# Performance work log

Hardware: AMD Instinct MI355X
Metric: run time of the kernel (lower is better)

The kernel has to match this reference:

```python
import jax, jax.numpy as jnp
import numpy as np

N_NODES = 100000
N_EDGES = 1600000
IN_F, HID_F, OUT_F = 128, 128, 64


def _sage_conv(x, src, dst, W_self, W_neigh, b, n_nodes):
    # DGL SAGEConv 'mean': out = x @ W_self + mean_{u in N(v)} x_u @ W_neigh + b
    agg = jax.ops.segment_sum(x[src], dst, num_segments=n_nodes)  # [N, d]
    deg = jax.ops.segment_sum(jnp.ones_like(dst, dtype=x.dtype), dst, num_segments=n_nodes)
    neigh = agg / jnp.maximum(deg, 1.0)[:, None]  # zero-in-degree nodes -> 0
    return x @ W_self + neigh @ W_neigh + b


def setup_inputs() -> dict:
    key = jax.random.key(0)
    ks = jax.random.split(key, 8)
    return {
        "features": jax.random.normal(ks[0], (N_NODES, IN_F), dtype=jnp.float32),
        "edge_src": jax.random.randint(ks[1], (N_EDGES,), 0, N_NODES, dtype=jnp.int32),
        "edge_dst": jax.random.randint(ks[2], (N_EDGES,), 0, N_NODES, dtype=jnp.int32),
        "W1_self": jax.random.normal(ks[3], (IN_F, HID_F), dtype=jnp.float32) / np.sqrt(IN_F),
        "W1_neigh": jax.random.normal(ks[4], (IN_F, HID_F), dtype=jnp.float32) / np.sqrt(IN_F),
        "b1": jnp.zeros((HID_F,), dtype=jnp.float32),
        "W2_self": jax.random.normal(ks[5], (HID_F, OUT_F), dtype=jnp.float32) / np.sqrt(HID_F),
        "W2_neigh": jax.random.normal(ks[6], (HID_F, OUT_F), dtype=jnp.float32) / np.sqrt(HID_F),
        "b2": jnp.zeros((OUT_F,), dtype=jnp.float32),
    }


def reference(features, edge_src, edge_dst, W1_self, W1_neigh, b1, W2_self, W2_neigh, b2):
    n = features.shape[0]
    x = _sage_conv(features, edge_src, edge_dst, W1_self, W1_neigh, b1, n)
    x = jax.nn.relu(x)
    # dropout with training=False is a no-op
    return _sage_conv(x, edge_src, edge_dst, W2_self, W2_neigh, b2, n)
```

## Files before the change

### kernel.cpp

```cpp
#include <hip/hip_runtime.h>

#define NODES 100000
#define EDGES 1600000
#define BSH 8
#define NBUCK ((NODES + 255) >> BSH)
#define CHUNK 4096
#define LMAX 8192
#define MCHUNKS ((NODES + 31) / 32)

using bf16x8 = __attribute__((ext_vector_type(8))) short;
using f32x4  = __attribute__((ext_vector_type(4))) float;
using f32x2  = __attribute__((ext_vector_type(2))) float;

__device__ __forceinline__ unsigned short f2b(float f) {
    unsigned u = __builtin_bit_cast(unsigned, f);
    unsigned r = (u + 0x7FFFu + ((u >> 16) & 1u)) >> 16;
    return (unsigned short)r;
}

__device__ __forceinline__ f32x2 pkadd(f32x2 a, f32x2 b) {
    f32x2 d;
    asm("v_pk_add_f32 %0, %1, %2" : "=v"(d) : "v"(a), "v"(b));
    return d;
}
__device__ __forceinline__ f32x2 pkfma(f32x2 a, f32x2 b, f32x2 c) {
    f32x2 d;
    asm("v_pk_fma_f32 %0, %1, %2, %3" : "=v"(d) : "v"(a), "v"(b), "v"(c));
    return d;
}
__device__ __forceinline__ unsigned cvt2bf(float lo, float hi) {
    unsigned r;
    asm("v_cvt_pk_bf16_f32 %0, %1, %2" : "=v"(r) : "v"(lo), "v"(hi));
    return r;
}

__device__ __forceinline__ void addpk8(f32x2* a, uint2 v) {
    a[0] = pkadd(a[0], __builtin_amdgcn_cvt_pk_f32_fp8((int)v.x, false));
    a[1] = pkadd(a[1], __builtin_amdgcn_cvt_pk_f32_fp8((int)v.x, true));
    a[2] = pkadd(a[2], __builtin_amdgcn_cvt_pk_f32_fp8((int)v.y, false));
    a[3] = pkadd(a[3], __builtin_amdgcn_cvt_pk_f32_fp8((int)v.y, true));
}


__global__ __launch_bounds__(256) void bhist_kernel(const int* __restrict__ dst,
                                                    int* __restrict__ bucket_cnt) {
    __shared__ int lcnt[512];
    int t = threadIdx.x;
    lcnt[t] = 0; lcnt[t + 256] = 0;
    __syncthreads();
    int base = blockIdx.x * 16384;
    int n = EDGES - base;
    if (n > 16384) n = 16384;
    const int4* d4 = reinterpret_cast<const int4*>(dst + base);
    for (int i = t; i < (n >> 2); i += 256) {
        int4 d = d4[i];
        atomicAdd(&lcnt[d.x >> BSH], 1);
        atomicAdd(&lcnt[d.y >> BSH], 1);
        atomicAdd(&lcnt[d.z >> BSH], 1);
        atomicAdd(&lcnt[d.w >> BSH], 1);
    }
    for (int i = (n & ~3) + t; i < n; i += 256) atomicAdd(&lcnt[dst[base + i] >> BSH], 1);
    __syncthreads();
    if (lcnt[t]) atomicAdd(&bucket_cnt[t], lcnt[t]);
    if (lcnt[t + 256]) atomicAdd(&bucket_cnt[t + 256], lcnt[t + 256]);
}

__global__ void bscan_kernel(const int* __restrict__ bucket_cnt, int* __restrict__ bucket_off,
                             int* __restrict__ gcursor, int* __restrict__ row_ptr) {
    __shared__ int sh[512];
    int t = threadIdx.x;
    int v = (t < NBUCK) ? bucket_cnt[t] : 0;
    sh[t] = v;
    __syncthreads();
    for (int off = 1; off < 512; off <<= 1) {
        int x = (t >= off) ? sh[t - off] : 0;
        __syncthreads();
        sh[t] += x;
        __syncthreads();
    }
    int excl = sh[t] - v;
    if (t < NBUCK) { bucket_off[t] = excl; gcursor[t] = excl; }
    if (t == NBUCK) bucket_off[t] = EDGES;
    if (t == 0) row_ptr[NODES] = EDGES;
}

__global__ __launch_bounds__(256) void binscat_kernel(
    const int* __restrict__ src, const int* __restrict__ dst,
    int* __restrict__ gcursor, unsigned* __restrict__ pairs) {
    __shared__ int cnt[512];
    __shared__ int scn[512];
    __shared__ int gbs[512];
    __shared__ int cur[512];
    __shared__ uint2 stage[CHUNK];
    int t = threadIdx.x;
    int base = blockIdx.x * CHUNK;
    int n = EDGES - base;
    if (n > CHUNK) n = CHUNK;

    cnt[t] = 0; cnt[t + 256] = 0;
    __syncthreads();

    uint2 my[16];
#pragma unroll
    for (int i = 0; i < 16; ++i) {
        int idx = t + i * 256;
        if (idx < n) {
            int d = dst[base + idx];
            int s = src[base + idx];
            my[i] = make_uint2((unsigned)d, (unsigned)s);
            atomicAdd(&cnt[d >> BSH], 1);
        } else {
            my[i] = make_uint2(0xFFFFFFFFu, 0);
        }
    }
    __syncthreads();
    scn[t] = cnt[t]; scn[t + 256] = cnt[t + 256];
    __syncthreads();
    for (int off = 1; off < 512; off <<= 1) {
        int a0 = (t >= off) ? scn[t - off] : 0;
        int a1 = (t + 256 >= off) ? scn[t + 256 - off] : 0;
        __syncthreads();
        scn[t] += a0; scn[t + 256] += a1;
        __syncthreads();
    }
    cur[t] = scn[t] - cnt[t];
    cur[t + 256] = scn[t + 256] - cnt[t + 256];
    __syncthreads();
#pragma unroll
    for (int i = 0; i < 16; ++i) {
        if (my[i].x != 0xFFFFFFFFu) {
            int b = (int)(my[i].x >> BSH);
            int p = atomicAdd(&cur[b], 1);
            stage[p] = my[i];
        }
    }
    for (int b2 = t; b2 < 512; b2 += 256) {
        int c = cnt[b2];
        gbs[b2] = (c > 0 && b2 < NBUCK) ? atomicAdd(&gcursor[b2], c) : 0;
    }
    __syncthreads();
    for (int idx = t; idx < n; idx += 256) {
        uint2 p = stage[idx];
        int b = (int)(p.x >> BSH);
        int excl = scn[b] - cnt[b];
        pairs[gbs[b] + idx - excl] = ((p.x & 255u) << 24) | p.y;
    }
}

__global__ __launch_bounds__(256) void localsort_kernel(
    const unsigned* __restrict__ pairs, const int* __restrict__ bucket_off,
    int* __restrict__ row_ptr, int* __restrict__ src_sorted) {
    __shared__ int cnt[256];
    __shared__ int cur[256];
    __shared__ int stage[LMAX];
    int b = blockIdx.x;
    int t = threadIdx.x;
    int node0 = b << BSH;
    int pbeg = bucket_off[b], pend = bucket_off[b + 1];
    int n = pend - pbeg;
    cnt[t] = 0;
    __syncthreads();
    for (int e = pbeg + t; e < pend; e += 256)
        atomicAdd(&cnt[(int)(pairs[e] >> 24)], 1);
    __syncthreads();
    int v = cnt[t];
    cur[t] = v;
    __syncthreads();
    for (int off = 1; off < 256; off <<= 1) {
        int x = (t >= off) ? cur[t - off] : 0;
        __syncthreads();
        cur[t] += x;
        __syncthreads();
    }
    int excl = cur[t] - v;
    int node = node0 + t;
    if (node < NODES) row_ptr[node] = pbeg + excl;
    cur[t] = excl;
    __syncthreads();
    if (n <= LMAX) {
        for (int e = pbeg + t; e < pend; e += 256) {
            unsigned p = pairs[e];
            int pos = atomicAdd(&cur[(int)(p >> 24)], 1);
            stage[pos] = (int)(p & 0xFFFFFFu);
        }
        __syncthreads();
        for (int i = t; i < n; i += 256) src_sorted[pbeg + i] = stage[i];
    } else {
        for (int e = pbeg + t; e < pend; e += 256) {
            unsigned p = pairs[e];
            int pos = atomicAdd(&cur[(int)(p >> 24)], 1);
            src_sorted[pbeg + pos] = (int)(p & 0xFFFFFFu);
        }
    }
}


__global__ void conv_kernel(const float* __restrict__ in, unsigned short* __restrict__ outb,
                            unsigned char* __restrict__ outq, int n4,
                            const float* __restrict__ W1s, const float* __restrict__ W1n,
                            const float* __restrict__ W2s, const float* __restrict__ W2n,
                            unsigned short* __restrict__ Wt1s, unsigned short* __restrict__ Wt1n,
                            unsigned short* __restrict__ Wt2s, unsigned short* __restrict__ Wt2n) {
    int i = blockIdx.x * 256 + threadIdx.x;
    if (i < n4) {
        float4 v = reinterpret_cast<const float4*>(in)[i];
        uint2 o;
        o.x = (unsigned)f2b(v.x) | ((unsigned)f2b(v.y) << 16);
        o.y = (unsigned)f2b(v.z) | ((unsigned)f2b(v.w) << 16);
        reinterpret_cast<uint2*>(outb)[i] = o;
        int pk = __builtin_amdgcn_cvt_pk_fp8_f32(v.x, v.y, 0, false);
        pk = __builtin_amdgcn_cvt_pk_fp8_f32(v.z, v.w, pk, true);
        reinterpret_cast<unsigned*>(outq)[i] = (unsigned)pk;
    }
    if (i < 16384) {
        int k = i >> 7, n = i & 127;
        Wt1s[n * 128 + k] = f2b(W1s[i]);
        Wt1n[n * 128 + k] = f2b(W1n[i]);
    }
    if (i < 8192) {
        int k = i >> 6, n = i & 63;
        Wt2s[n * 128 + k] = f2b(W2s[i]);
        Wt2n[n * 128 + k] = f2b(W2n[i]);
    }
}


__global__ __launch_bounds__(256) void agg128_fp8(
    const unsigned char* __restrict__ xq, const int* __restrict__ row_ptr,
    const int* __restrict__ srcs, unsigned short* __restrict__ out) {
    int w = (blockIdx.x * 256 + threadIdx.x) >> 6;
    int lane = threadIdx.x & 63;
    if (w >= NODES) return;
    int g = lane >> 4;
    int sl = lane & 15;
    int beg = row_ptr[w], end = row_ptr[w + 1];

    f32x2 A0[4], A1[4];
#pragma unroll
    for (int i = 0; i < 4; ++i) { A0[i] = {0.f, 0.f}; A1[i] = {0.f, 0.f}; }

    const unsigned char* xs = xq + sl * 8;
    int e = beg + g;
    for (; e + 12 < end; e += 16) {
        int s0 = srcs[e];
        int s1 = srcs[e + 4];
        int s2 = srcs[e + 8];
        int s3 = srcs[e + 12];
        uint2 v0 = *reinterpret_cast<const uint2*>(xs + (size_t)s0 * 128);
        uint2 v1 = *reinterpret_cast<const uint2*>(xs + (size_t)s1 * 128);
        uint2 v2 = *reinterpret_cast<const uint2*>(xs + (size_t)s2 * 128);
        uint2 v3 = *reinterpret_cast<const uint2*>(xs + (size_t)s3 * 128);
        addpk8(A0, v0);
        addpk8(A1, v1);
        addpk8(A0, v2);
        addpk8(A1, v3);
    }
    for (; e + 4 < end; e += 8) {
        int s0 = srcs[e];
        int s1 = srcs[e + 4];
        uint2 v0 = *reinterpret_cast<const uint2*>(xs + (size_t)s0 * 128);
        uint2 v1 = *reinterpret_cast<const uint2*>(xs + (size_t)s1 * 128);
        addpk8(A0, v0);
        addpk8(A1, v1);
    }
    if (e < end) {
        int s0 = srcs[e];
        uint2 v0 = *reinterpret_cast<const uint2*>(xs + (size_t)s0 * 128);
        addpk8(A0, v0);
    }

#pragma unroll
    for (int i = 0; i < 4; ++i) {
        f32x2 s = pkadd(A0[i], A1[i]);
        f32x2 t;
        t[0] = __shfl_xor(s[0], 16, 64);
        t[1] = __shfl_xor(s[1], 16, 64);
        s = pkadd(s, t);
        t[0] = __shfl_xor(s[0], 32, 64);
        t[1] = __shfl_xor(s[1], 32, 64);
        A0[i] = pkadd(s, t);
    }
    if (g == 0) {
        float inv = 1.0f / fmaxf((float)(end - beg), 1.0f);
        uint4 o;
        o.x = cvt2bf(A0[0][0] * inv, A0[0][1] * inv);
        o.y = cvt2bf(A0[1][0] * inv, A0[1][1] * inv);
        o.z = cvt2bf(A0[2][0] * inv, A0[2][1] * inv);
        o.w = cvt2bf(A0[3][0] * inv, A0[3][1] * inv);
        *reinterpret_cast<uint4*>(out + (size_t)w * 128 + sl * 8) = o;
    }
}

__global__ __launch_bounds__(256) void agg64_add8(
    const unsigned char* __restrict__ xq, const int* __restrict__ row_ptr,
    const int* __restrict__ srcs, float* __restrict__ out) {
    int w = (blockIdx.x * 256 + threadIdx.x) >> 6;
    int lane = threadIdx.x & 63;
    if (w >= NODES) return;
    int g = lane >> 3;
    int sl = lane & 7;
    int beg = row_ptr[w], end = row_ptr[w + 1];

    f32x2 A0[4], A1[4];
#pragma unroll
    for (int i = 0; i < 4; ++i) { A0[i] = {0.f, 0.f}; A1[i] = {0.f, 0.f}; }

    const unsigned char* xs = xq + sl * 8;
    int e = beg + g;
    for (; e + 8 < end; e += 16) {
        int s0 = srcs[e];
        int s1 = srcs[e + 8];
        uint2 v0 = *reinterpret_cast<const uint2*>(xs + (size_t)s0 * 64);
        uint2 v1 = *reinterpret_cast<const uint2*>(xs + (size_t)s1 * 64);
        addpk8(A0, v0);
        addpk8(A1, v1);
    }
    if (e < end) {
        int s0 = srcs[e];
        uint2 v0 = *reinterpret_cast<const uint2*>(xs + (size_t)s0 * 64);
        addpk8(A0, v0);
    }
#pragma unroll
    for (int i = 0; i < 4; ++i) {
        f32x2 s = pkadd(A0[i], A1[i]);
        f32x2 t;
        t[0] = __shfl_xor(s[0], 8, 64);
        t[1] = __shfl_xor(s[1], 8, 64);
        s = pkadd(s, t);
        t[0] = __shfl_xor(s[0], 16, 64);
        t[1] = __shfl_xor(s[1], 16, 64);
        s = pkadd(s, t);
        t[0] = __shfl_xor(s[0], 32, 64);
        t[1] = __shfl_xor(s[1], 32, 64);
        A0[i] = pkadd(s, t);
    }
    if (g == 0) {
        float inv = 1.0f / fmaxf((float)(end - beg), 1.0f);
        f32x2 iv = {inv, inv};
        f32x2* op = reinterpret_cast<f32x2*>(out + (size_t)w * 64 + sl * 8);
        f32x2 r0 = op[0], r1 = op[1], r2 = op[2], r3 = op[3];
        op[0] = pkfma(A0[0], iv, r0);
        op[1] = pkfma(A0[1], iv, r1);
        op[2] = pkfma(A0[2], iv, r2);
        op[3] = pkfma(A0[3], iv, r3);
    }
}


__global__ __launch_bounds__(256, 2) void fused_mlp(
    const unsigned short* __restrict__ featb, const unsigned short* __restrict__ agg,
    const unsigned short* __restrict__ Wt1s, const unsigned short* __restrict__ Wt1n,
    const float* __restrict__ b1, const unsigned short* __restrict__ Wt2s,
    const unsigned short* __restrict__ Wt2n, const float* __restrict__ b2,
    unsigned char* __restrict__ x1h8, float* __restrict__ outp) {
    __shared__ __align__(16) unsigned short x1t[2][32 * 136];
    int wid = threadIdx.x >> 6, lane = threadIdx.x & 63;
    int l15 = lane & 15, quad = lane >> 4;

    bf16x8 B1s[2][4], B1n[2][4];
#pragma unroll
    for (int nt = 0; nt < 2; ++nt) {
        int col = wid * 32 + nt * 16 + l15;
#pragma unroll
        for (int k = 0; k < 4; ++k) {
            B1s[nt][k] = *reinterpret_cast<const bf16x8*>(Wt1s + (size_t)col * 128 + k * 32 + quad * 8);
            B1n[nt][k] = *reinterpret_cast<const bf16x8*>(Wt1n + (size_t)col * 128 + k * 32 + quad * 8);
        }
    }
    bf16x8 B2s[4], B2n[4];
    int col2 = wid * 16 + l15;
#pragma unroll
    for (int k = 0; k < 4; ++k) {
        B2s[k] = *reinterpret_cast<const bf16x8*>(Wt2s + (size_t)col2 * 128 + k * 32 + quad * 8);
        B2n[k] = *reinterpret_cast<const bf16x8*>(Wt2n + (size_t)col2 * 128 + k * 32 + quad * 8);
    }
    float bv1[2];
    bv1[0] = b1[wid * 32 + l15];
    bv1[1] = b1[wid * 32 + 16 + l15];
    float bv2 = b2[col2];

    auto loadA = [&](int cc, bf16x8 (&Afd)[2][4], bf16x8 (&Aad)[2][4]) {
#pragma unroll
        for (int rg = 0; rg < 2; ++rg) {
            int r = cc * 32 + rg * 16 + l15;
            if (r >= NODES) r = NODES - 1;
            const unsigned short* fp = featb + (size_t)r * 128 + quad * 8;
            const unsigned short* ap = agg + (size_t)r * 128 + quad * 8;
#pragma unroll
            for (int k = 0; k < 4; ++k) {
                Afd[rg][k] = *reinterpret_cast<const bf16x8*>(fp + k * 32);
                Aad[rg][k] = *reinterpret_cast<const bf16x8*>(ap + k * 32);
            }
        }
    };

    bf16x8 Af[2][4], Aa[2][4];
    int c = blockIdx.x;
    if (c < MCHUNKS) loadA(c, Af, Aa);
    int buf = 0;
    for (; c < MCHUNKS; c += gridDim.x) {
        int rbase = c * 32;
        int cn = c + (int)gridDim.x;

        f32x4 acc[2][2];
#pragma unroll
        for (int rg = 0; rg < 2; ++rg)
#pragma unroll
            for (int nt = 0; nt < 2; ++nt) acc[rg][nt] = {0.f, 0.f, 0.f, 0.f};
#pragma unroll
        for (int k = 0; k < 4; ++k)
#pragma unroll
            for (int nt = 0; nt < 2; ++nt)
#pragma unroll
                for (int rg = 0; rg < 2; ++rg) {
                    acc[rg][nt] = __builtin_amdgcn_mfma_f32_16x16x32_bf16(Af[rg][k], B1s[nt][k], acc[rg][nt], 0, 0, 0);
                    acc[rg][nt] = __builtin_amdgcn_mfma_f32_16x16x32_bf16(Aa[rg][k], B1n[nt][k], acc[rg][nt], 0, 0, 0);
                }

        bf16x8 Pf[2][4], Pa[2][4];
        if (cn < MCHUNKS) loadA(cn, Pf, Pa);

#pragma unroll
        for (int nt = 0; nt < 2; ++nt)
#pragma unroll
            for (int rg = 0; rg < 2; ++rg)
#pragma unroll
                for (int rr = 0; rr < 4; ++rr) {
                    float v = fmaxf(acc[rg][nt][rr] + bv1[nt], 0.f);
                    x1t[buf][(rg * 16 + quad * 4 + rr) * 136 + wid * 32 + nt * 16 + l15] = f2b(v);
                }
        __syncthreads();

        f32x4 acc2s[2], acc2n[2];
#pragma unroll
        for (int rg = 0; rg < 2; ++rg) { acc2s[rg] = {0.f, 0.f, 0.f, 0.f}; acc2n[rg] = {0.f, 0.f, 0.f, 0.f}; }
#pragma unroll
        for (int k = 0; k < 4; ++k)
#pragma unroll
            for (int rg = 0; rg < 2; ++rg) {
                bf16x8 a = *reinterpret_cast<const bf16x8*>(&x1t[buf][(rg * 16 + l15) * 136 + k * 32 + quad * 8]);
                acc2s[rg] = __builtin_amdgcn_mfma_f32_16x16x32_bf16(a, B2s[k], acc2s[rg], 0, 0, 0);
                acc2n[rg] = __builtin_amdgcn_mfma_f32_16x16x32_bf16(a, B2n[k], acc2n[rg], 0, 0, 0);
            }
#pragma unroll
        for (int rg = 0; rg < 2; ++rg)
#pragma unroll
            for (int rr = 0; rr < 4; ++rr) {
                int row = rbase + rg * 16 + quad * 4 + rr;
                if (row < NODES) {
                    float vn = acc2n[rg][rr];
                    int pk = __builtin_amdgcn_cvt_pk_fp8_f32(vn, vn, 0, false);
                    x1h8[(size_t)row * 64 + col2] = (unsigned char)(pk & 0xFF);
                    outp[(size_t)row * 64 + col2] = acc2s[rg][rr] + bv2;
                }
            }

        buf ^= 1;
        if (cn < MCHUNKS) {
#pragma unroll
            for (int rg = 0; rg < 2; ++rg)
#pragma unroll
                for (int k = 0; k < 4; ++k) {
                    Af[rg][k] = Pf[rg][k];
                    Aa[rg][k] = Pa[rg][k];
                }
        }
    }
}


extern "C" void kernel_launch(void* const* d_in, const int* in_sizes, int n_in,
                              void* d_out, int out_size, void* d_ws, size_t ws_size,
                              hipStream_t stream) {
    const float* features = (const float*)d_in[0];
    const int* esrc = (const int*)d_in[1];
    const int* edst = (const int*)d_in[2];
    const float* W1s = (const float*)d_in[3];
    const float* W1n = (const float*)d_in[4];
    const float* b1  = (const float*)d_in[5];
    const float* W2s = (const float*)d_in[6];
    const float* W2n = (const float*)d_in[7];
    const float* b2  = (const float*)d_in[8];
    float* out = (float*)d_out;

    char* ws = (char*)d_ws;
    size_t off = 0;
    auto alloc = [&](size_t bytes) {
        void* p = ws + off;
        off += (bytes + 255) & ~(size_t)255;
        return p;
    };
    int* bucket_cnt = (int*)alloc(512 * 4);
    int* bucket_off = (int*)alloc(512 * 4);
    int* gcursor    = (int*)alloc(512 * 4);
    int* row_ptr    = (int*)alloc((size_t)(NODES + 1) * 4);
    int* src_sorted = (int*)alloc((size_t)EDGES * 4);
    unsigned* pairs = (unsigned*)alloc((size_t)EDGES * 4);
    unsigned short* featb = (unsigned short*)alloc((size_t)NODES * 128 * 2);
    unsigned char*  feat8 = (unsigned char*)alloc((size_t)NODES * 128);
    unsigned short* agg1  = (unsigned short*)alloc((size_t)NODES * 128 * 2);
    unsigned char*  x1h8  = (unsigned char*)alloc((size_t)NODES * 64);
    unsigned short* Wt1s  = (unsigned short*)alloc(16384 * 2);
    unsigned short* Wt1n  = (unsigned short*)alloc(16384 * 2);
    unsigned short* Wt2s  = (unsigned short*)alloc(8192 * 2);
    unsigned short* Wt2n  = (unsigned short*)alloc(8192 * 2);

    conv_kernel<<<(NODES * 128 / 4 + 255) / 256, 256, 0, stream>>>(
        features, featb, feat8, NODES * 128 / 4, W1s, W1n, W2s, W2n, Wt1s, Wt1n, Wt2s, Wt2n);

    hipMemsetAsync(bucket_cnt, 0, 512 * 4, stream);
    bhist_kernel<<<(EDGES + 16383) / 16384, 256, 0, stream>>>(edst, bucket_cnt);
    bscan_kernel<<<1, 512, 0, stream>>>(bucket_cnt, bucket_off, gcursor, row_ptr);
    binscat_kernel<<<(EDGES + CHUNK - 1) / CHUNK, 256, 0, stream>>>(esrc, edst, gcursor, pairs);
    localsort_kernel<<<NBUCK, 256, 0, stream>>>(pairs, bucket_off, row_ptr, src_sorted);

    agg128_fp8<<<(NODES * 64 + 255) / 256, 256, 0, stream>>>(feat8, row_ptr, src_sorted, agg1);

    fused_mlp<<<1024, 256, 0, stream>>>(featb, agg1, Wt1s, Wt1n, b1, Wt2s, Wt2n, b2, x1h8, out);

    agg64_add8<<<(NODES * 64 + 255) / 256, 256, 0, stream>>>(x1h8, row_ptr, src_sorted, out);
}
```

Baseline: 286.3 us.

## Map multiple nodes per wave in aggregation and fuse conversion with histogram

The aggregation kernels now give each wave 4 nodes (128-wide layer) or 8 nodes (64-wide layer) instead of one. Each lane group loads a batch of source indices cooperatively and broadcasts them with shuffles, which removes the cross-group shuffle reductions. Out-of-range edges are padded to a zeroed dummy row, so the gather needs no branch. Separately, the feature and weight conversion kernel is merged into the edge histogram kernel as one launch. The cost is that lane groups inside a wave now diverge when node degrees differ, and two small memsets are added for the padding rows.

```diff
diff --git a/kernel.cpp b/kernel.cpp
--- a/kernel.cpp
+++ b/kernel.cpp
@@ -7,6 +7,7 @@
 #define CHUNK 4096
 #define LMAX 8192
 #define MCHUNKS ((NODES + 31) / 32)
+#define CONVB 12500
 
 using bf16x8 = __attribute__((ext_vector_type(8))) short;
 using f32x4  = __attribute__((ext_vector_type(4))) float;
@@ -42,13 +43,43 @@
 }
 
 
-__global__ __launch_bounds__(256) void bhist_kernel(const int* __restrict__ dst,
-                                                    int* __restrict__ bucket_cnt) {
+__global__ __launch_bounds__(256) void conv_hist(
+    const float* __restrict__ in, unsigned short* __restrict__ outb,
+    unsigned char* __restrict__ outq, int n4,
+    const float* __restrict__ W1s, const float* __restrict__ W1n,
+    const float* __restrict__ W2s, const float* __restrict__ W2n,
+    unsigned short* __restrict__ Wt1s, unsigned short* __restrict__ Wt1n,
+    unsigned short* __restrict__ Wt2s, unsigned short* __restrict__ Wt2n,
+    const int* __restrict__ dst, int* __restrict__ bucket_cnt) {
+    int t = threadIdx.x;
+    if (blockIdx.x < CONVB) {
+        int i = blockIdx.x * 256 + t;
+        if (i < n4) {
+            float4 v = reinterpret_cast<const float4*>(in)[i];
+            uint2 o;
+            o.x = (unsigned)f2b(v.x) | ((unsigned)f2b(v.y) << 16);
+            o.y = (unsigned)f2b(v.z) | ((unsigned)f2b(v.w) << 16);
+            reinterpret_cast<uint2*>(outb)[i] = o;
+            int pk = __builtin_amdgcn_cvt_pk_fp8_f32(v.x, v.y, 0, false);
+            pk = __builtin_amdgcn_cvt_pk_fp8_f32(v.z, v.w, pk, true);
+            reinterpret_cast<unsigned*>(outq)[i] = (unsigned)pk;
+        }
+        if (i < 16384) {
+            int k = i >> 7, n = i & 127;
+            Wt1s[n * 128 + k] = f2b(W1s[i]);
+            Wt1n[n * 128 + k] = f2b(W1n[i]);
+        }
+        if (i < 8192) {
+            int k = i >> 6, n = i & 63;
+            Wt2s[n * 128 + k] = f2b(W2s[i]);
+            Wt2n[n * 128 + k] = f2b(W2n[i]);
+        }
+        return;
+    }
     __shared__ int lcnt[512];
-    int t = threadIdx.x;
     lcnt[t] = 0; lcnt[t + 256] = 0;
     __syncthreads();
-    int base = blockIdx.x * 16384;
+    int base = (blockIdx.x - CONVB) * 16384;
     int n = EDGES - base;
     if (n > 16384) n = 16384;
     const int4* d4 = reinterpret_cast<const int4*>(dst + base);
@@ -195,155 +226,101 @@
 }
 
 
-__global__ void conv_kernel(const float* __restrict__ in, unsigned short* __restrict__ outb,
-                            unsigned char* __restrict__ outq, int n4,
-                            const float* __restrict__ W1s, const float* __restrict__ W1n,
-                            const float* __restrict__ W2s, const float* __restrict__ W2n,
-                            unsigned short* __restrict__ Wt1s, unsigned short* __restrict__ Wt1n,
-                            unsigned short* __restrict__ Wt2s, unsigned short* __restrict__ Wt2n) {
-    int i = blockIdx.x * 256 + threadIdx.x;
-    if (i < n4) {
-        float4 v = reinterpret_cast<const float4*>(in)[i];
-        uint2 o;
-        o.x = (unsigned)f2b(v.x) | ((unsigned)f2b(v.y) << 16);
-        o.y = (unsigned)f2b(v.z) | ((unsigned)f2b(v.w) << 16);
-        reinterpret_cast<uint2*>(outb)[i] = o;
-        int pk = __builtin_amdgcn_cvt_pk_fp8_f32(v.x, v.y, 0, false);
-        pk = __builtin_amdgcn_cvt_pk_fp8_f32(v.z, v.w, pk, true);
-        reinterpret_cast<unsigned*>(outq)[i] = (unsigned)pk;
-    }
-    if (i < 16384) {
-        int k = i >> 7, n = i & 127;
-        Wt1s[n * 128 + k] = f2b(W1s[i]);
-        Wt1n[n * 128 + k] = f2b(W1n[i]);
-    }
-    if (i < 8192) {
-        int k = i >> 6, n = i & 63;
-        Wt2s[n * 128 + k] = f2b(W2s[i]);
-        Wt2n[n * 128 + k] = f2b(W2n[i]);
-    }
-}
-
-
 __global__ __launch_bounds__(256) void agg128_fp8(
     const unsigned char* __restrict__ xq, const int* __restrict__ row_ptr,
     const int* __restrict__ srcs, unsigned short* __restrict__ out) {
-    int w = (blockIdx.x * 256 + threadIdx.x) >> 6;
+    int wave = (blockIdx.x * 256 + threadIdx.x) >> 6;
     int lane = threadIdx.x & 63;
-    if (w >= NODES) return;
-    int g = lane >> 4;
     int sl = lane & 15;
-    int beg = row_ptr[w], end = row_ptr[w + 1];
+    int n = wave * 4 + (lane >> 4);
+    if (n >= NODES) return;
+    int beg = row_ptr[n], end = row_ptr[n + 1];
+    int gb = lane & 48;
 
     f32x2 A0[4], A1[4];
 #pragma unroll
     for (int i = 0; i < 4; ++i) { A0[i] = {0.f, 0.f}; A1[i] = {0.f, 0.f}; }
 
     const unsigned char* xs = xq + sl * 8;
-    int e = beg + g;
-    for (; e + 12 < end; e += 16) {
-        int s0 = srcs[e];
-        int s1 = srcs[e + 4];
-        int s2 = srcs[e + 8];
-        int s3 = srcs[e + 12];
-        uint2 v0 = *reinterpret_cast<const uint2*>(xs + (size_t)s0 * 128);
-        uint2 v1 = *reinterpret_cast<const uint2*>(xs + (size_t)s1 * 128);
-        uint2 v2 = *reinterpret_cast<const uint2*>(xs + (size_t)s2 * 128);
-        uint2 v3 = *reinterpret_cast<const uint2*>(xs + (size_t)s3 * 128);
-        addpk8(A0, v0);
-        addpk8(A1, v1);
-        addpk8(A0, v2);
-        addpk8(A1, v3);
-    }
-    for (; e + 4 < end; e += 8) {
-        int s0 = srcs[e];
-        int s1 = srcs[e + 4];
-        uint2 v0 = *reinterpret_cast<const uint2*>(xs + (size_t)s0 * 128);
-        uint2 v1 = *reinterpret_cast<const uint2*>(xs + (size_t)s1 * 128);
-        addpk8(A0, v0);
-        addpk8(A1, v1);
-    }
-    if (e < end) {
-        int s0 = srcs[e];
-        uint2 v0 = *reinterpret_cast<const uint2*>(xs + (size_t)s0 * 128);
-        addpk8(A0, v0);
-    }
-
-#pragma unroll
-    for (int i = 0; i < 4; ++i) {
-        f32x2 s = pkadd(A0[i], A1[i]);
-        f32x2 t;
-        t[0] = __shfl_xor(s[0], 16, 64);
-        t[1] = __shfl_xor(s[1], 16, 64);
-        s = pkadd(s, t);
-        t[0] = __shfl_xor(s[0], 32, 64);
-        t[1] = __shfl_xor(s[1], 32, 64);
-        A0[i] = pkadd(s, t);
-    }
-    if (g == 0) {
-        float inv = 1.0f / fmaxf((float)(end - beg), 1.0f);
-        uint4 o;
-        o.x = cvt2bf(A0[0][0] * inv, A0[0][1] * inv);
-        o.y = cvt2bf(A0[1][0] * inv, A0[1][1] * inv);
-        o.z = cvt2bf(A0[2][0] * inv, A0[2][1] * inv);
-        o.w = cvt2bf(A0[3][0] * inv, A0[3][1] * inv);
-        *reinterpret_cast<uint4*>(out + (size_t)w * 128 + sl * 8) = o;
-    }
+    for (int base = beg; base < end; base += 16) {
+        int idx = base + sl;
+        int sv = (idx < end) ? srcs[idx] : NODES;
+        uint2 vv[8], ww[8];
+#pragma unroll
+        for (int j = 0; j < 8; ++j) {
+            int s = __shfl(sv, gb + j, 64);
+            vv[j] = *reinterpret_cast<const uint2*>(xs + (size_t)s * 128);
+        }
+#pragma unroll
+        for (int j = 0; j < 8; ++j) {
+            int s = __shfl(sv, gb + 8 + j, 64);
+            ww[j] = *reinterpret_cast<const uint2*>(xs + (size_t)s * 128);
+        }
+#pragma unroll
+        for (int j = 0; j < 8; ++j) addpk8((j & 1) ? A1 : A0, vv[j]);
+#pragma unroll
+        for (int j = 0; j < 8; ++j) addpk8((j & 1) ? A0 : A1, ww[j]);
+    }
+
+    float inv = 1.0f / fmaxf((float)(end - beg), 1.0f);
+    f32x2 iv = {inv, inv};
+    f32x2 z = {0.f, 0.f};
+    f32x2 r0 = pkfma(pkadd(A0[0], A1[0]), iv, z);
+    f32x2 r1 = pkfma(pkadd(A0[1], A1[1]), iv, z);
+    f32x2 r2 = pkfma(pkadd(A0[2], A1[2]), iv, z);
+    f32x2 r3 = pkfma(pkadd(A0[3], A1[3]), iv, z);
+    uint4 o;
+    o.x = cvt2bf(r0[0], r0[1]);
+    o.y = cvt2bf(r1[0], r1[1]);
+    o.z = cvt2bf(r2[0], r2[1]);
+    o.w = cvt2bf(r3[0], r3[1]);
+    *reinterpret_cast<uint4*>(out + (size_t)n * 128 + sl * 8) = o;
 }
 
 __global__ __launch_bounds__(256) void agg64_add8(
     const unsigned char* __restrict__ xq, const int* __restrict__ row_ptr,
     const int* __restrict__ srcs, float* __restrict__ out) {
-    int w = (blockIdx.x * 256 + threadIdx.x) >> 6;
+    int wave = (blockIdx.x * 256 + threadIdx.x) >> 6;
     int lane = threadIdx.x & 63;
-    if (w >= NODES) return;
-    int g = lane >> 3;
     int sl = lane & 7;
-    int beg = row_ptr[w], end = row_ptr[w + 1];
+    int n = wave * 8 + (lane >> 3);
+    if (n >= NODES) return;
+    int beg = row_ptr[n], end = row_ptr[n + 1];
+    int gb = lane & 56;
 
     f32x2 A0[4], A1[4];
 #pragma unroll
     for (int i = 0; i < 4; ++i) { A0[i] = {0.f, 0.f}; A1[i] = {0.f, 0.f}; }
 
     const unsigned char* xs = xq + sl * 8;
-    int e = beg + g;
-    for (; e + 8 < end; e += 16) {
-        int s0 = srcs[e];
-        int s1 = srcs[e + 8];
-        uint2 v0 = *reinterpret_cast<const uint2*>(xs + (size_t)s0 * 64);
-        uint2 v1 = *reinterpret_cast<const uint2*>(xs + (size_t)s1 * 64);
-        addpk8(A0, v0);
-        addpk8(A1, v1);
-    }
-    if (e < end) {
-        int s0 = srcs[e];
-        uint2 v0 = *reinterpret_cast<const uint2*>(xs + (size_t)s0 * 64);
-        addpk8(A0, v0);
-    }
-#pragma unroll
-    for (int i = 0; i < 4; ++i) {
-        f32x2 s = pkadd(A0[i], A1[i]);
-        f32x2 t;
-        t[0] = __shfl_xor(s[0], 8, 64);
-        t[1] = __shfl_xor(s[1], 8, 64);
-        s = pkadd(s, t);
-        t[0] = __shfl_xor(s[0], 16, 64);
-        t[1] = __shfl_xor(s[1], 16, 64);
-        s = pkadd(s, t);
-        t[0] = __shfl_xor(s[0], 32, 64);
-        t[1] = __shfl_xor(s[1], 32, 64);
-        A0[i] = pkadd(s, t);
-    }
-    if (g == 0) {
-        float inv = 1.0f / fmaxf((float)(end - beg), 1.0f);
-        f32x2 iv = {inv, inv};
-        f32x2* op = reinterpret_cast<f32x2*>(out + (size_t)w * 64 + sl * 8);
-        f32x2 r0 = op[0], r1 = op[1], r2 = op[2], r3 = op[3];
-        op[0] = pkfma(A0[0], iv, r0);
-        op[1] = pkfma(A0[1], iv, r1);
-        op[2] = pkfma(A0[2], iv, r2);
-        op[3] = pkfma(A0[3], iv, r3);
-    }
+    for (int base = beg; base < end; base += 8) {
+        int idx = base + sl;
+        int sv = (idx < end) ? srcs[idx] : NODES;
+        uint2 vv[8];
+#pragma unroll
+        for (int j = 0; j < 8; ++j) {
+            int s = __shfl(sv, gb + j, 64);
+            vv[j] = *reinterpret_cast<const uint2*>(xs + (size_t)s * 64);
+        }
+#pragma unroll
+        for (int j = 0; j < 8; ++j) addpk8((j & 1) ? A1 : A0, vv[j]);
+    }
+
+    float inv = 1.0f / fmaxf((float)(end - beg), 1.0f);
+    f32x2 iv = {inv, inv};
+    float* op = out + (size_t)n * 64 + sl * 8;
+    f32x2 r0 = *reinterpret_cast<f32x2*>(op);
+    f32x2 r1 = *reinterpret_cast<f32x2*>(op + 2);
+    f32x2 r2 = *reinterpret_cast<f32x2*>(op + 4);
+    f32x2 r3 = *reinterpret_cast<f32x2*>(op + 6);
+    r0 = pkfma(pkadd(A0[0], A1[0]), iv, r0);
+    r1 = pkfma(pkadd(A0[1], A1[1]), iv, r1);
+    r2 = pkfma(pkadd(A0[2], A1[2]), iv, r2);
+    r3 = pkfma(pkadd(A0[3], A1[3]), iv, r3);
+    *reinterpret_cast<f32x2*>(op) = r0;
+    *reinterpret_cast<f32x2*>(op + 2) = r1;
+    *reinterpret_cast<f32x2*>(op + 4) = r2;
+    *reinterpret_cast<f32x2*>(op + 6) = r3;
 }
 
 
@@ -497,26 +474,29 @@
     int* src_sorted = (int*)alloc((size_t)EDGES * 4);
     unsigned* pairs = (unsigned*)alloc((size_t)EDGES * 4);
     unsigned short* featb = (unsigned short*)alloc((size_t)NODES * 128 * 2);
-    unsigned char*  feat8 = (unsigned char*)alloc((size_t)NODES * 128);
+    unsigned char*  feat8 = (unsigned char*)alloc((size_t)(NODES + 1) * 128);
     unsigned short* agg1  = (unsigned short*)alloc((size_t)NODES * 128 * 2);
-    unsigned char*  x1h8  = (unsigned char*)alloc((size_t)NODES * 64);
+    unsigned char*  x1h8  = (unsigned char*)alloc((size_t)(NODES + 1) * 64);
     unsigned short* Wt1s  = (unsigned short*)alloc(16384 * 2);
     unsigned short* Wt1n  = (unsigned short*)alloc(16384 * 2);
     unsigned short* Wt2s  = (unsigned short*)alloc(8192 * 2);
     unsigned short* Wt2n  = (unsigned short*)alloc(8192 * 2);
 
-    conv_kernel<<<(NODES * 128 / 4 + 255) / 256, 256, 0, stream>>>(
-        features, featb, feat8, NODES * 128 / 4, W1s, W1n, W2s, W2n, Wt1s, Wt1n, Wt2s, Wt2n);
-
     hipMemsetAsync(bucket_cnt, 0, 512 * 4, stream);
-    bhist_kernel<<<(EDGES + 16383) / 16384, 256, 0, stream>>>(edst, bucket_cnt);
+    hipMemsetAsync(feat8 + (size_t)NODES * 128, 0, 128, stream);
+    hipMemsetAsync(x1h8 + (size_t)NODES * 64, 0, 64, stream);
+
+    conv_hist<<<CONVB + (EDGES + 16383) / 16384, 256, 0, stream>>>(
+        features, featb, feat8, NODES * 128 / 4, W1s, W1n, W2s, W2n,
+        Wt1s, Wt1n, Wt2s, Wt2n, edst, bucket_cnt);
+
     bscan_kernel<<<1, 512, 0, stream>>>(bucket_cnt, bucket_off, gcursor, row_ptr);
     binscat_kernel<<<(EDGES + CHUNK - 1) / CHUNK, 256, 0, stream>>>(esrc, edst, gcursor, pairs);
     localsort_kernel<<<NBUCK, 256, 0, stream>>>(pairs, bucket_off, row_ptr, src_sorted);
 
-    agg128_fp8<<<(NODES * 64 + 255) / 256, 256, 0, stream>>>(feat8, row_ptr, src_sorted, agg1);
+    agg128_fp8<<<(NODES / 4 * 64 + 255) / 256, 256, 0, stream>>>(feat8, row_ptr, src_sorted, agg1);
 
     fused_mlp<<<1024, 256, 0, stream>>>(featb, agg1, Wt1s, Wt1n, b1, Wt2s, Wt2n, b2, x1h8, out);
 
-    agg64_add8<<<(NODES * 64 + 255) / 256, 256, 0, stream>>>(x1h8, row_ptr, src_sorted, out);
-}
+    agg64_add8<<<(NODES / 8 * 64 + 255) / 256, 256, 0, stream>>>(x1h8, row_ptr, src_sorted, out);
+}
```

Result: faster. 259.2 us (-9.5%).
